# Performance work log

Hardware: AMD Instinct MI355X
Metric: run time of the kernel (lower is better)

The kernel has to match this reference:

```python
import jax, jax.numpy as jnp
import numpy as np

N = 10000          # nodes
E = 160000         # edges
T = 32             # seq_len == n_timesteps
H = 256            # hidden_size
K = 4              # edge_embedding_dim
NF = T * 6         # node_features
PRED = 8           # predicted_timesteps
T_TEACH = T - PRED # teacher-forced steps


def setup_inputs() -> dict:
    key = jax.random.key(0)
    ks = jax.random.split(key, 16)
    s = 0.05
    return {
        "x": jax.random.normal(ks[0], (N, NF), jnp.float32),
        "edge_index": jax.random.randint(ks[1], (2, E), 0, N, jnp.int64),
        "z": jax.random.uniform(ks[2], (E, K), jnp.float32),
        # inner f_out: Linear(H, NF) + ReLU
        "Wf": jax.random.normal(ks[3], (H, NF), jnp.float32) * s,
        "bf": jax.random.normal(ks[4], (NF,), jnp.float32) * s,
        # k-1 edge MLPs: Linear(2*NF, H) -> ReLU -> Linear(H, H), stacked
        "W1": jax.random.normal(ks[5], (K - 1, 2 * NF, H), jnp.float32) * s,
        "b1": jax.random.normal(ks[6], (K - 1, H), jnp.float32) * s,
        "W2": jax.random.normal(ks[7], (K - 1, H, H), jnp.float32) * s,
        "b2": jax.random.normal(ks[8], (K - 1, H), jnp.float32) * s,
        # GRUCell(6, H): torch gate order r, z, n
        "Wih": jax.random.normal(ks[9], (3 * H, 6), jnp.float32) * s,
        "bih": jax.random.normal(ks[10], (3 * H,), jnp.float32) * s,
        "Whh": jax.random.normal(ks[11], (3 * H, H), jnp.float32) * s,
        "bhh": jax.random.normal(ks[12], (3 * H,), jnp.float32) * s,
        # outer f_out: Linear(H, 6) + ReLU
        "Wo": jax.random.normal(ks[13], (H, 6), jnp.float32) * s,
        "bo": jax.random.normal(ks[14], (6,), jnp.float32) * s,
    }


def _forward(x, edge_index, z, Wf, bf, W1, b1, W2, b2, Wih, bih, Whh, bhh, Wo, bo):
    src = edge_index[0]  # x_j (source)
    dst = edge_index[1]  # x_i (target, aggregation index)
    zw = z[:, 1:K].T[:, :, None]  # [K-1, E, 1]
    ones_e = jnp.ones((E,), x.dtype)
    cnt = jnp.maximum(jax.ops.segment_sum(ones_e, dst, num_segments=N), 1.0)[:, None]

    def step(carry, inp):
        h, prev = carry
        t, x_t = inp
        inputs = jnp.where(t < T_TEACH, x_t, prev)  # [N, 6]
        fh = jax.nn.relu(h @ Wf + bf)               # [N, NF]
        # message: cat([x_i, x_j]) = [target, source], detached in torch
        ef = jax.lax.stop_gradient(
            jnp.concatenate([fh[dst], fh[src]], axis=1))  # [E, 2*NF]
        h1 = jax.nn.relu(jnp.einsum('ef,kfh->keh', ef, W1) + b1[:, None, :])
        h2 = jnp.einsum('keh,khg->keg', h1, W2) + b2[:, None, :]  # [K-1,E,H]
        msg = jnp.sum(zw * h2, axis=0)              # [E, H]
        m = jax.ops.segment_sum(msg, dst, num_segments=N) / cnt  # scatter-mean
        # GRUCell(inputs, hidden=m)
        gx = inputs @ Wih.T + bih                   # [N, 3H]
        gh = m @ Whh.T + bhh                        # [N, 3H]
        rx, zx, nx = jnp.split(gx, 3, axis=1)
        rh, zh, nh = jnp.split(gh, 3, axis=1)
        r = jax.nn.sigmoid(rx + rh)
        zg = jax.nn.sigmoid(zx + zh)
        n = jnp.tanh(nx + r * nh)
        h_new = (1.0 - zg) * n + zg * m             # [N, H]
        mu = inputs + jax.nn.relu(h_new @ Wo + bo)  # [N, 6]
        return (h_new, mu), mu

    x_seq = x.reshape(N, T, 6).transpose(1, 0, 2)   # [T, N, 6]
    ts = jnp.arange(T)
    h0 = jnp.zeros((N, H), x.dtype)
    p0 = jnp.zeros((N, 6), x.dtype)
    _, mus = jax.lax.scan(step, (h0, p0), (ts, x_seq))  # [T, N, 6]
    return mus.transpose(1, 0, 2).reshape(N, NF)


def reference(x, edge_index, z, Wf, bf, W1, b1, W2, b2, Wih, bih, Whh, bhh, Wo, bo):
    return _forward(x, edge_index, z, Wf, bf, W1, b1, W2, b2,
                    Wih, bih, Whh, bhh, Wo, bo)
```

## Files before the change

### kernel.cpp

```cpp
#include <hip/hip_runtime.h>
#include <hip/hip_bf16.h>

#define NN 10000
#define NE 160000
#define TS 32
#define HID 256
#define NFEAT 192
#define TTEACH 24

typedef unsigned short u16;
typedef unsigned int u32;
typedef __attribute__((ext_vector_type(8))) short bf16x8;
typedef __attribute__((ext_vector_type(4))) float f32x4;

__device__ __forceinline__ float bf2f(u16 u){
    u32 v = ((u32)u) << 16;
    union { u32 i; float f; } c; c.i = v; return c.f;
}
__device__ __forceinline__ u16 f2bf(float f){
    union { float f; u32 i; } c; c.f = f;
    u32 i = c.i;
    u32 lsb = (i >> 16) & 1u;
    i += 0x7fffu + lsb;
    return (u16)(i >> 16);
}

__global__ void fill_f32(float* p, float v, int n){
    int i = blockIdx.x * 256 + threadIdx.x;
    if (i < n) p[i] = v;
}
__global__ void fill_i32(int* p, int v, int n){
    int i = blockIdx.x * 256 + threadIdx.x;
    if (i < n) p[i] = v;
}
__global__ void copy_i32(const int* __restrict__ a, int* __restrict__ b, int n){
    int i = blockIdx.x * 256 + threadIdx.x;
    if (i < n) b[i] = a[i];
}

__global__ void detect_f32(const u16* __restrict__ zraw, int* __restrict__ flag){
    int c = 0;
    for (int i = 0; i < 128; i++) if (zraw[2*i] >= 0x4000) c++;
    *flag = (c > 8) ? 1 : 0;
}
__global__ void conv_f32(const void* __restrict__ in, float* __restrict__ outp,
                         int n, const int* __restrict__ flag){
    int i = blockIdx.x * 256 + threadIdx.x;
    if (i >= n) return;
    if (*flag) outp[i] = ((const float*)in)[i];
    else       outp[i] = bf2f(((const u16*)in)[i]);
}
__global__ void detect_i64(const int* __restrict__ ei_raw, int* __restrict__ flag){
    int zz = 0;
    #pragma unroll
    for (int i = 0; i < 32; i++) zz |= ei_raw[2*i + 1];
    *flag = (zz == 0) ? 1 : 0;
}
__global__ void copy_edges(const int* __restrict__ ei_raw, const int* __restrict__ flag,
                           int* __restrict__ src, int* __restrict__ dst){
    int e = blockIdx.x * 256 + threadIdx.x;
    if (e >= NE) return;
    int st = (*flag) ? 2 : 1;
    src[e] = ei_raw[(size_t)e * st];
    dst[e] = ei_raw[((size_t)NE + e) * st];
}

__global__ void degree_k(const int* __restrict__ dst, int* __restrict__ cnt, int n){
    int e = blockIdx.x * 256 + threadIdx.x;
    if (e < n) atomicAdd(&cnt[dst[e]], 1);
}
__global__ void invcnt_k(const int* __restrict__ cnt, float* __restrict__ inv, int n){
    int i = blockIdx.x * 256 + threadIdx.x;
    if (i < n) inv[i] = 1.0f / fmaxf((float)cnt[i], 1.0f);
}

__global__ void scan_k(const int* __restrict__ cnt, int* __restrict__ binoff){
    __shared__ int ps[1024];
    int t = threadIdx.x;
    int s = 0;
    if (t < 1000)
        for (int i = 0; i < 10; i++) s += cnt[t*10 + i];
    ps[t] = s;
    __syncthreads();
    for (int ofs = 1; ofs < 1024; ofs <<= 1){
        int v = (t >= ofs) ? ps[t - ofs] : 0;
        __syncthreads();
        ps[t] += v;
        __syncthreads();
    }
    if (t < 1000){
        int run = (t == 0) ? 0 : ps[t-1];
        for (int i = 0; i < 10; i++){
            binoff[t*10 + i] = run;
            run += cnt[t*10 + i];
        }
    }
}
__global__ void scatter_k(const int* __restrict__ src32, const int* __restrict__ dst32,
                          const float* __restrict__ zc, int* __restrict__ cur,
                          int* __restrict__ srcS, int* __restrict__ dstS,
                          float* __restrict__ zS){
    int e = blockIdx.x * 256 + threadIdx.x;
    if (e >= NE) return;
    int d = dst32[e];
    int pos = atomicAdd(&cur[d], 1);
    srcS[pos] = src32[e];
    dstS[pos] = d;
    zS[pos]        = zc[(size_t)e*4 + 1];
    zS[NE + pos]   = zc[(size_t)e*4 + 2];
    zS[2*NE + pos] = zc[(size_t)e*4 + 3];
}

__global__ void build_wft(const float* __restrict__ Wfc, u16* __restrict__ WfT){
    int idx = blockIdx.x * 256 + threadIdx.x;
    if (idx < 256 * 192){
        int k = idx / 192, n = idx % 192;
        WfT[(size_t)n * 256 + k] = f2bf(Wfc[idx]);
    }
}
__global__ void build_w1t(const float* __restrict__ W1c, u16* __restrict__ W1T){
    int idx = blockIdx.x * 256 + threadIdx.x;
    if (idx < 1536 * 192){
        int n = idx / 192, k = idx % 192;
        int kblk = n >> 9, part = (n >> 8) & 1, c = n & 255;
        W1T[idx] = f2bf(W1c[(size_t)kblk * (384*256) + (size_t)(part*192 + k) * 256 + c]);
    }
}
__global__ void conv_bf16(const float* __restrict__ in, u16* __restrict__ outp, int n){
    int i = blockIdx.x * 256 + threadIdx.x;
    if (i < n) outp[i] = f2bf(in[i]);
}
__global__ void build_w2t(const float* __restrict__ W2c, u16* __restrict__ W2T){
    int idx = blockIdx.x * 256 + threadIdx.x;
    if (idx < 768 * 256){
        int k = idx / 256, n = idx % 256;
        W2T[(size_t)n * 768 + k] = f2bf(W2c[idx]);
    }
}
__global__ void mscale_k(float* __restrict__ m_acc, const float* __restrict__ inv,
                         u16* __restrict__ m16){
    int idx = blockIdx.x * 256 + threadIdx.x;
    if (idx < NN * HID){
        m16[idx] = f2bf(m_acc[idx] * inv[idx >> 8]);
        m_acc[idx] = 0.f;
    }
}

template<int MODE>
__global__ __launch_bounds__(256, 2) void gemm_mfma(
    const u16* __restrict__ A16, const u16* __restrict__ BT16,
    const float* __restrict__ bias, float* __restrict__ Cf, u16* __restrict__ Cb,
    int M, int Kd, int Nd)
{
    __shared__ __align__(16) u16 Alds[256 * 40];
    __shared__ __align__(16) u16 Blds[64 * 40];
    const int tid = threadIdx.x;
    const int m0 = blockIdx.x * 256;
    const int n0 = blockIdx.y * 64;
    const int wave = tid >> 6, lane = tid & 63;
    const int quad = lane >> 4, l16 = lane & 15;

    const f32x4 zero4 = {0.f, 0.f, 0.f, 0.f};
    f32x4 acc[4][4];
    #pragma unroll
    for (int r=0;r<4;r++)
        #pragma unroll
        for (int c=0;c<4;c++) acc[r][c] = zero4;

    const int arow = m0 + tid;
    const u16* ap = &A16[(size_t)arow * Kd];
    const int bn = tid >> 2, bseg = tid & 3;
    const u16* bp = &BT16[(size_t)(n0 + bn) * Kd + bseg * 8];

    for (int k0 = 0; k0 < Kd; k0 += 32){
        if (arow < M){
            const uint4* q = reinterpret_cast<const uint4*>(ap + k0);
            uint4 v0 = q[0], v1 = q[1], v2 = q[2], v3 = q[3];
            *reinterpret_cast<uint4*>(&Alds[tid * 40])      = v0;
            *reinterpret_cast<uint4*>(&Alds[tid * 40 + 8])  = v1;
            *reinterpret_cast<uint4*>(&Alds[tid * 40 + 16]) = v2;
            *reinterpret_cast<uint4*>(&Alds[tid * 40 + 24]) = v3;
        } else {
            uint4 zz = {0,0,0,0};
            #pragma unroll
            for (int s=0;s<4;s++)
                *reinterpret_cast<uint4*>(&Alds[tid * 40 + s*8]) = zz;
        }
        {
            uint4 v = *reinterpret_cast<const uint4*>(bp + k0);
            *reinterpret_cast<uint4*>(&Blds[bn * 40 + bseg * 8]) = v;
        }
        __syncthreads();
        bf16x8 af[4], bfr[4];
        #pragma unroll
        for (int r=0;r<4;r++)
            af[r] = *reinterpret_cast<const bf16x8*>(&Alds[(wave*64 + r*16 + l16) * 40 + quad * 8]);
        #pragma unroll
        for (int c=0;c<4;c++)
            bfr[c] = *reinterpret_cast<const bf16x8*>(&Blds[(c*16 + l16) * 40 + quad * 8]);
        #pragma unroll
        for (int r=0;r<4;r++)
            #pragma unroll
            for (int c=0;c<4;c++)
                acc[r][c] = __builtin_amdgcn_mfma_f32_16x16x32_bf16(af[r], bfr[c], acc[r][c], 0, 0, 0);
        __syncthreads();
    }
    #pragma unroll
    for (int c=0;c<4;c++){
        int col = n0 + c*16 + l16;
        float bv = 0.f;
        if (MODE == 0 || MODE == 2) bv = bias[col];
        if (MODE == 1){
            int part = (col >> 8) & 1;
            if (part == 0) bv = bias[(col >> 9) * 256 + (col & 255)];
        }
        #pragma unroll
        for (int r=0;r<4;r++){
            #pragma unroll
            for (int reg=0;reg<4;reg++){
                int row = m0 + wave*64 + r*16 + quad*4 + reg;
                if (row >= M) continue;
                float v = acc[r][c][reg] + bv;
                if (MODE == 0) v = fmaxf(v, 0.f);
                if (MODE == 2) Cf[(size_t)row * Nd + col] = v;
                else           Cb[(size_t)row * Nd + col] = f2bf(v);
            }
        }
    }
}

__global__ __launch_bounds__(256, 2) void edge_mfma(
    const u16* __restrict__ AB16, const u16* __restrict__ W2T,
    const float* __restrict__ b2, const float* __restrict__ zS,
    const int* __restrict__ srcS, const int* __restrict__ dstS,
    float* __restrict__ m_acc)
{
    __shared__ __align__(16) char smem[33280];
    u16*   Alds = (u16*)smem;
    u16*   Blds = (u16*)(smem + 5120);
    float* stg  = (float*)smem;
    __shared__ float zc3[3][64];
    __shared__ int dstc[64], srcc[64];
    const int tid = threadIdx.x;
    const int eb = blockIdx.x * 64;

    if (tid < 64){
        srcc[tid] = srcS[eb + tid];
        dstc[tid] = dstS[eb + tid];
    }
    int tz = tid - 64;
    if (tz >= 0 && tz < 192){
        int g = tz / 64, e = tz % 64;
        zc3[g][e] = zS[(size_t)g * NE + eb + e];
    }
    __syncthreads();

    const int wave = tid >> 6, lane = tid & 63;
    const int quad = lane >> 4, l16 = lane & 15;
    const int est = tid >> 2, seg = tid & 3;

    const f32x4 zero4 = {0.f, 0.f, 0.f, 0.f};
    f32x4 acc[4][4];
    #pragma unroll
    for (int r=0;r<4;r++)
        #pragma unroll
        for (int c=0;c<4;c++) acc[r][c] = zero4;

    const int d = dstc[est], s = srcc[est];
    const u16* paB = &AB16[(size_t)d * 1536];
    const u16* pbB = &AB16[(size_t)s * 1536 + 256];
    const int bn = tid >> 2;
    const u16* bwB = &W2T[(size_t)bn * 768 + seg * 8];

    uint4 pa = *reinterpret_cast<const uint4*>(&paB[seg * 8]);
    uint4 pb = *reinterpret_cast<const uint4*>(&pbB[seg * 8]);

    for (int kc = 0; kc < 768; kc += 32){
        const int g = kc >> 8;
        {
            const u16* wa = (const u16*)&pa;
            const u16* wb = (const u16*)&pb;
            float zk = zc3[g][est];
            u16 pk[8];
            #pragma unroll
            for (int i=0;i<8;i++){
                float v = zk * fmaxf(bf2f(wa[i]) + bf2f(wb[i]), 0.f);
                pk[i] = f2bf(v);
            }
            *reinterpret_cast<uint4*>(&Alds[est * 40 + seg * 8]) = *reinterpret_cast<uint4*>(pk);
        }
        #pragma unroll
        for (int i=0;i<4;i++){
            uint4 w = *reinterpret_cast<const uint4*>(&bwB[(size_t)i * 64 * 768 + kc]);
            *reinterpret_cast<uint4*>(&Blds[(bn + i*64) * 40 + seg * 8]) = w;
        }
        __syncthreads();
        if (kc + 32 < 768){
            const int kn = kc + 32;
            const int gn = kn >> 8;
            const int jn = (kn & 255) + seg * 8;
            pa = *reinterpret_cast<const uint4*>(&paB[gn * 512 + jn]);
            pb = *reinterpret_cast<const uint4*>(&pbB[gn * 512 + jn]);
        }
        bf16x8 af[4], bfr[4];
        #pragma unroll
        for (int r=0;r<4;r++)
            af[r] = *reinterpret_cast<const bf16x8*>(&Alds[(r*16 + l16) * 40 + quad * 8]);
        #pragma unroll
        for (int c=0;c<4;c++)
            bfr[c] = *reinterpret_cast<const bf16x8*>(&Blds[(wave*64 + c*16 + l16) * 40 + quad * 8]);
        #pragma unroll
        for (int r=0;r<4;r++)
            #pragma unroll
            for (int c=0;c<4;c++)
                acc[r][c] = __builtin_amdgcn_mfma_f32_16x16x32_bf16(af[r], bfr[c], acc[r][c], 0, 0, 0);
        __syncthreads();
    }
    #pragma unroll
    for (int c=0;c<4;c++){
        int col = wave*64 + c*16 + l16;
        float b20 = b2[col], b21 = b2[256 + col], b22 = b2[512 + col];
        #pragma unroll
        for (int r=0;r<4;r++){
            #pragma unroll
            for (int reg=0;reg<4;reg++){
                int e = r*16 + quad*4 + reg;
                acc[r][c][reg] += zc3[0][e]*b20 + zc3[1][e]*b21 + zc3[2][e]*b22;
            }
        }
    }
    float sum = 0.f;
    int cur_d = -1;
    const int colg = wave*64 + lane;
    #pragma unroll
    for (int chunk = 0; chunk < 2; chunk++){
        #pragma unroll
        for (int rr = 0; rr < 2; rr++){
            int r = chunk*2 + rr;
            #pragma unroll
            for (int c=0;c<4;c++)
                #pragma unroll
                for (int reg=0;reg<4;reg++){
                    int el = rr*16 + quad*4 + reg;
                    stg[wave*(32*65) + el*65 + c*16 + l16] = acc[r][c][reg];
                }
        }
        __syncthreads();
        for (int e = 0; e < 32; e++){
            int eg = chunk*32 + e;
            int dn = dstc[eg];
            float v = stg[wave*(32*65) + e*65 + lane];
            if (dn != cur_d){
                if (cur_d >= 0) atomicAdd(&m_acc[(size_t)cur_d * 256 + colg], sum);
                cur_d = dn; sum = v;
            } else {
                sum += v;
            }
        }
        __syncthreads();
    }
    if (cur_d >= 0) atomicAdd(&m_acc[(size_t)cur_d * 256 + colg], sum);
}

__global__ void gates_mu_k(
    const float* __restrict__ gh, const u16* __restrict__ m16,
    const float* __restrict__ x, const float* __restrict__ Wih,
    const float* __restrict__ bih, const float* __restrict__ Wo,
    const float* __restrict__ bo, float* __restrict__ prev,
    u16* __restrict__ h16, void* __restrict__ out,
    const int* __restrict__ flag, int t)
{
    const int n = blockIdx.x;
    const int j = threadIdx.x;
    const int idx = n * 256 + j;
    float inp[6];
    if (t < TTEACH){
        #pragma unroll
        for (int c=0;c<6;c++) inp[c] = x[(size_t)n * NFEAT + t * 6 + c];
    } else {
        #pragma unroll
        for (int c=0;c<6;c++) inp[c] = prev[n * 6 + c];
    }
    float m = bf2f(m16[idx]);
    float gxr = bih[j], gxz = bih[256 + j], gxn = bih[512 + j];
    #pragma unroll
    for (int c=0;c<6;c++){
        gxr += inp[c] * Wih[j * 6 + c];
        gxz += inp[c] * Wih[(256 + j) * 6 + c];
        gxn += inp[c] * Wih[(512 + j) * 6 + c];
    }
    float ghr = gh[(size_t)n * 768 + j];
    float ghz = gh[(size_t)n * 768 + 256 + j];
    float ghn = gh[(size_t)n * 768 + 512 + j];
    float r  = 1.f / (1.f + __expf(-(gxr + ghr)));
    float zg = 1.f / (1.f + __expf(-(gxz + ghz)));
    float nn = tanhf(gxn + r * ghn);
    float hv = (1.f - zg) * nn + zg * m;
    h16[idx] = f2bf(hv);
    __shared__ float hl[256];
    __shared__ float part[6][9];
    hl[j] = hv;
    __syncthreads();
    if (j < 48){
        int c = j >> 3, p = j & 7;
        float s = 0.f;
        #pragma unroll 8
        for (int q = 0; q < 32; q++){
            int jj = p*32 + q;
            s += hl[jj] * Wo[jj * 6 + c];
        }
        part[c][p] = s;
    }
    __syncthreads();
    if (j < 6){
        float s = bo[j];
        #pragma unroll
        for (int p = 0; p < 8; p++) s += part[j][p];
        float mu = inp[j] + fmaxf(s, 0.f);
        if (*flag) ((float*)out)[(size_t)n * NFEAT + t * 6 + j] = mu;
        else       ((u16*)out)[(size_t)n * NFEAT + t * 6 + j] = f2bf(mu);
        prev[n * 6 + j] = mu;
    }
}

extern "C" void kernel_launch(void* const* d_in, const int* in_sizes, int n_in,
                              void* d_out, int out_size, void* d_ws, size_t ws_size,
                              hipStream_t stream)
{
    const void* x_r   = d_in[0];
    const int*  ei    = (const int*)d_in[1];
    const void* z_r   = d_in[2];
    const void* Wf_r  = d_in[3];
    const void* bf_r  = d_in[4];
    const void* W1_r  = d_in[5];
    const void* b1_r  = d_in[6];
    const void* W2_r  = d_in[7];
    const void* b2_r  = d_in[8];
    const void* Wih_r = d_in[9];
    const void* bih_r = d_in[10];
    const void* Whh_r = d_in[11];
    const void* bhh_r = d_in[12];
    const void* Wo_r  = d_in[13];
    const void* bo_r  = d_in[14];

    char* ws = (char*)d_ws;
    size_t off = 0;
    auto alloc = [&](size_t bytes){
        void* p = ws + off;
        off += (bytes + 255) & ~(size_t)255;
        return p;
    };
    u16*   h16   = (u16*)  alloc((size_t)NN * HID * 2);
    float* prev  = (float*)alloc((size_t)NN * 6 * 4);
    u16*   fh16  = (u16*)  alloc((size_t)NN * NFEAT * 2);
    u16*   AB16  = (u16*)  alloc((size_t)NN * 1536 * 2);
    float* m_acc = (float*)alloc((size_t)NN * HID * 4);
    u16*   m16   = (u16*)  alloc((size_t)NN * HID * 2);
    float* gh    = (float*)alloc((size_t)NN * 768 * 4);
    float* invc  = (float*)alloc((size_t)NN * 4);
    int*   cnt   = (int*)  alloc((size_t)NN * 4);
    int*   binoff= (int*)  alloc((size_t)(NN + 1) * 4);
    int*   curw  = (int*)  alloc((size_t)NN * 4);
    u16*   WfT   = (u16*)  alloc((size_t)192 * 256 * 2);
    u16*   W1T   = (u16*)  alloc((size_t)1536 * 192 * 2);
    u16*   Whh16 = (u16*)  alloc((size_t)768 * 256 * 2);
    u16*   W2T   = (u16*)  alloc((size_t)256 * 768 * 2);
    int*   src32 = (int*)  alloc((size_t)NE * 4);
    int*   dst32 = (int*)  alloc((size_t)NE * 4);
    int*   srcS  = (int*)  alloc((size_t)NE * 4);
    int*   dstS  = (int*)  alloc((size_t)NE * 4);
    float* zS    = (float*)alloc((size_t)3 * NE * 4);
    int*   fdt   = (int*)  alloc(256);
    int*   fidx  = (int*)  alloc(256);
    float* xc   = (float*)alloc((size_t)NN * NFEAT * 4);
    float* zc   = (float*)alloc((size_t)NE * 4 * 4);
    float* Wfc  = (float*)alloc((size_t)256 * 192 * 4);
    float* bfc  = (float*)alloc(192 * 4);
    float* W1c  = (float*)alloc((size_t)3 * 384 * 256 * 4);
    float* b1c  = (float*)alloc(768 * 4);
    float* W2c  = (float*)alloc((size_t)3 * 256 * 256 * 4);
    float* b2c  = (float*)alloc(768 * 4);
    float* Wihc = (float*)alloc((size_t)768 * 6 * 4);
    float* bihc = (float*)alloc(768 * 4);
    float* Whhc = (float*)alloc((size_t)768 * 256 * 4);
    float* bhhc = (float*)alloc(768 * 4);
    float* Woc  = (float*)alloc((size_t)256 * 6 * 4);
    float* boc  = (float*)alloc(6 * 4);

    detect_f32<<<1, 1, 0, stream>>>((const u16*)z_r, fdt);
    detect_i64<<<1, 1, 0, stream>>>(ei, fidx);
    copy_edges<<<(NE + 255)/256, 256, 0, stream>>>(ei, fidx, src32, dst32);

    auto conv = [&](const void* in, float* outp, int n){
        conv_f32<<<(n + 255)/256, 256, 0, stream>>>(in, outp, n, fdt);
    };
    conv(x_r,   xc,   NN * NFEAT);
    conv(z_r,   zc,   NE * 4);
    conv(Wf_r,  Wfc,  256 * 192);
    conv(bf_r,  bfc,  192);
    conv(W1_r,  W1c,  3 * 384 * 256);
    conv(b1_r,  b1c,  768);
    conv(W2_r,  W2c,  3 * 256 * 256);
    conv(b2_r,  b2c,  768);
    conv(Wih_r, Wihc, 768 * 6);
    conv(bih_r, bihc, 768);
    conv(Whh_r, Whhc, 768 * 256);
    conv(bhh_r, bhhc, 768);
    conv(Wo_r,  Woc,  256 * 6);
    conv(bo_r,  boc,  6);

    fill_f32<<<(NN*HID/2 + 255)/256, 256, 0, stream>>>((float*)h16, 0.f, NN*HID/2);
    fill_f32<<<(NN*6 + 255)/256, 256, 0, stream>>>(prev, 0.f, NN*6);
    fill_f32<<<(NN*HID + 255)/256, 256, 0, stream>>>(m_acc, 0.f, NN*HID);
    fill_i32<<<(NN + 255)/256, 256, 0, stream>>>(cnt, 0, NN);
    degree_k<<<(NE + 255)/256, 256, 0, stream>>>(dst32, cnt, NE);
    invcnt_k<<<(NN + 255)/256, 256, 0, stream>>>(cnt, invc, NN);
    scan_k<<<1, 1024, 0, stream>>>(cnt, binoff);
    copy_i32<<<(NN + 255)/256, 256, 0, stream>>>(binoff, curw, NN);
    scatter_k<<<(NE + 255)/256, 256, 0, stream>>>(src32, dst32, zc, curw, srcS, dstS, zS);
    build_wft<<<(256*192 + 255)/256, 256, 0, stream>>>(Wfc, WfT);
    build_w1t<<<(1536*192 + 255)/256, 256, 0, stream>>>(W1c, W1T);
    conv_bf16<<<(768*256 + 255)/256, 256, 0, stream>>>(Whhc, Whh16, 768*256);
    build_w2t<<<(768*256 + 255)/256, 256, 0, stream>>>(W2c, W2T);

    for (int t = 0; t < TS; t++){
        gemm_mfma<0><<<dim3(40, 3), 256, 0, stream>>>(h16, WfT, bfc, nullptr, fh16, NN, 256, NFEAT);
        gemm_mfma<1><<<dim3(40, 24), 256, 0, stream>>>(fh16, W1T, b1c, nullptr, AB16, NN, NFEAT, 1536);
        edge_mfma<<<2500, 256, 0, stream>>>(AB16, W2T, b2c, zS, srcS, dstS, m_acc);
        mscale_k<<<(NN*HID + 255)/256, 256, 0, stream>>>(m_acc, invc, m16);
        gemm_mfma<2><<<dim3(40, 12), 256, 0, stream>>>(m16, Whh16, bhhc, gh, nullptr, NN, 256, 768);
        gates_mu_k<<<NN, 256, 0, stream>>>(gh, m16, xc, Wihc, bihc, Woc, boc, prev, h16, d_out, fdt, t);
    }
}
```

Baseline: 7.231 ms.

## Fuse mean-scaling into Whh GEMM and gates kernel, drop mscale pass

Removes the separate mscale kernel. The Whh GEMM now reads the fp32 scatter accumulator directly, scaling rows by inverse degree and converting to bf16 while loading tiles. The gates kernel reads fp32 m and resets the accumulator to zero. The edge kernel also uses packed bf16x2 conversions and a smaller 16-row staging chunk in its epilogue, which shrinks LDS use. The cost is that the GEMM A loads are twice as wide (fp32), and the gates kernel now uses fp32 m where it used bf16 before.

```diff
diff --git a/kernel.cpp b/kernel.cpp
--- a/kernel.cpp
+++ b/kernel.cpp
@@ -137,19 +137,12 @@
         W2T[(size_t)n * 768 + k] = f2bf(W2c[idx]);
     }
 }
-__global__ void mscale_k(float* __restrict__ m_acc, const float* __restrict__ inv,
-                         u16* __restrict__ m16){
-    int idx = blockIdx.x * 256 + threadIdx.x;
-    if (idx < NN * HID){
-        m16[idx] = f2bf(m_acc[idx] * inv[idx >> 8]);
-        m_acc[idx] = 0.f;
-    }
-}
 
 template<int MODE>
 __global__ __launch_bounds__(256, 2) void gemm_mfma(
     const u16* __restrict__ A16, const u16* __restrict__ BT16,
     const float* __restrict__ bias, float* __restrict__ Cf, u16* __restrict__ Cb,
+    const float* __restrict__ A32, const float* __restrict__ rowscale,
     int M, int Kd, int Nd)
 {
     __shared__ __align__(16) u16 Alds[256 * 40];
@@ -168,23 +161,50 @@
         for (int c=0;c<4;c++) acc[r][c] = zero4;
 
     const int arow = m0 + tid;
-    const u16* ap = &A16[(size_t)arow * Kd];
+    const u16* ap = (MODE == 2) ? nullptr : &A16[(size_t)arow * Kd];
     const int bn = tid >> 2, bseg = tid & 3;
     const u16* bp = &BT16[(size_t)(n0 + bn) * Kd + bseg * 8];
+    float rs = 0.f;
+    if (MODE == 2 && arow < M) rs = rowscale[arow];
 
     for (int k0 = 0; k0 < Kd; k0 += 32){
-        if (arow < M){
-            const uint4* q = reinterpret_cast<const uint4*>(ap + k0);
-            uint4 v0 = q[0], v1 = q[1], v2 = q[2], v3 = q[3];
-            *reinterpret_cast<uint4*>(&Alds[tid * 40])      = v0;
-            *reinterpret_cast<uint4*>(&Alds[tid * 40 + 8])  = v1;
-            *reinterpret_cast<uint4*>(&Alds[tid * 40 + 16]) = v2;
-            *reinterpret_cast<uint4*>(&Alds[tid * 40 + 24]) = v3;
+        if (MODE == 2){
+            if (arow < M){
+                const float4* q = reinterpret_cast<const float4*>(&A32[(size_t)arow * Kd + k0]);
+                u32 pk[16];
+                #pragma unroll
+                for (int s=0;s<8;s++){
+                    float4 v = q[s];
+                    float2 p0; p0.x = v.x * rs; p0.y = v.y * rs;
+                    float2 p1; p1.x = v.z * rs; p1.y = v.w * rs;
+                    __hip_bfloat162 h0 = __float22bfloat162_rn(p0);
+                    __hip_bfloat162 h1 = __float22bfloat162_rn(p1);
+                    pk[2*s]   = *reinterpret_cast<u32*>(&h0);
+                    pk[2*s+1] = *reinterpret_cast<u32*>(&h1);
+                }
+                #pragma unroll
+                for (int s=0;s<4;s++)
+                    *reinterpret_cast<uint4*>(&Alds[tid * 40 + s*8]) = *reinterpret_cast<uint4*>(&pk[4*s]);
+            } else {
+                uint4 zz = {0,0,0,0};
+                #pragma unroll
+                for (int s=0;s<4;s++)
+                    *reinterpret_cast<uint4*>(&Alds[tid * 40 + s*8]) = zz;
+            }
         } else {
-            uint4 zz = {0,0,0,0};
-            #pragma unroll
-            for (int s=0;s<4;s++)
-                *reinterpret_cast<uint4*>(&Alds[tid * 40 + s*8]) = zz;
+            if (arow < M){
+                const uint4* q = reinterpret_cast<const uint4*>(ap + k0);
+                uint4 v0 = q[0], v1 = q[1], v2 = q[2], v3 = q[3];
+                *reinterpret_cast<uint4*>(&Alds[tid * 40])      = v0;
+                *reinterpret_cast<uint4*>(&Alds[tid * 40 + 8])  = v1;
+                *reinterpret_cast<uint4*>(&Alds[tid * 40 + 16]) = v2;
+                *reinterpret_cast<uint4*>(&Alds[tid * 40 + 24]) = v3;
+            } else {
+                uint4 zz = {0,0,0,0};
+                #pragma unroll
+                for (int s=0;s<4;s++)
+                    *reinterpret_cast<uint4*>(&Alds[tid * 40 + s*8]) = zz;
+            }
         }
         {
             uint4 v = *reinterpret_cast<const uint4*>(bp + k0);
@@ -235,7 +255,7 @@
     const int* __restrict__ srcS, const int* __restrict__ dstS,
     float* __restrict__ m_acc)
 {
-    __shared__ __align__(16) char smem[33280];
+    __shared__ __align__(16) char smem[25600];
     u16*   Alds = (u16*)smem;
     u16*   Blds = (u16*)(smem + 5120);
     float* stg  = (float*)smem;
@@ -278,14 +298,19 @@
     for (int kc = 0; kc < 768; kc += 32){
         const int g = kc >> 8;
         {
-            const u16* wa = (const u16*)&pa;
-            const u16* wb = (const u16*)&pb;
+            union { uint4 v; u32 w[4]; } UA, UB;
+            UA.v = pa; UB.v = pb;
             float zk = zc3[g][est];
-            u16 pk[8];
+            u32 pk[4];
             #pragma unroll
-            for (int i=0;i<8;i++){
-                float v = zk * fmaxf(bf2f(wa[i]) + bf2f(wb[i]), 0.f);
-                pk[i] = f2bf(v);
+            for (int i=0;i<4;i++){
+                float2 fa = __bfloat1622float2(*reinterpret_cast<__hip_bfloat162*>(&UA.w[i]));
+                float2 fb = __bfloat1622float2(*reinterpret_cast<__hip_bfloat162*>(&UB.w[i]));
+                float2 v;
+                v.x = zk * fmaxf(fa.x + fb.x, 0.f);
+                v.y = zk * fmaxf(fa.y + fb.y, 0.f);
+                __hip_bfloat162 hr = __float22bfloat162_rn(v);
+                pk[i] = *reinterpret_cast<u32*>(&hr);
             }
             *reinterpret_cast<uint4*>(&Alds[est * 40 + seg * 8]) = *reinterpret_cast<uint4*>(pk);
         }
@@ -333,23 +358,17 @@
     int cur_d = -1;
     const int colg = wave*64 + lane;
     #pragma unroll
-    for (int chunk = 0; chunk < 2; chunk++){
-        #pragma unroll
-        for (int rr = 0; rr < 2; rr++){
-            int r = chunk*2 + rr;
+    for (int r = 0; r < 4; r++){
+        #pragma unroll
+        for (int c=0;c<4;c++)
             #pragma unroll
-            for (int c=0;c<4;c++)
-                #pragma unroll
-                for (int reg=0;reg<4;reg++){
-                    int el = rr*16 + quad*4 + reg;
-                    stg[wave*(32*65) + el*65 + c*16 + l16] = acc[r][c][reg];
-                }
-        }
-        __syncthreads();
-        for (int e = 0; e < 32; e++){
-            int eg = chunk*32 + e;
+            for (int reg=0;reg<4;reg++)
+                stg[wave*(16*65) + (quad*4 + reg)*65 + c*16 + l16] = acc[r][c][reg];
+        __syncthreads();
+        for (int e = 0; e < 16; e++){
+            int eg = r*16 + e;
             int dn = dstc[eg];
-            float v = stg[wave*(32*65) + e*65 + lane];
+            float v = stg[wave*(16*65) + e*65 + lane];
             if (dn != cur_d){
                 if (cur_d >= 0) atomicAdd(&m_acc[(size_t)cur_d * 256 + colg], sum);
                 cur_d = dn; sum = v;
@@ -363,11 +382,11 @@
 }
 
 __global__ void gates_mu_k(
-    const float* __restrict__ gh, const u16* __restrict__ m16,
-    const float* __restrict__ x, const float* __restrict__ Wih,
-    const float* __restrict__ bih, const float* __restrict__ Wo,
-    const float* __restrict__ bo, float* __restrict__ prev,
-    u16* __restrict__ h16, void* __restrict__ out,
+    const float* __restrict__ gh, float* __restrict__ m_acc,
+    const float* __restrict__ inv_cnt, const float* __restrict__ x,
+    const float* __restrict__ Wih, const float* __restrict__ bih,
+    const float* __restrict__ Wo, const float* __restrict__ bo,
+    float* __restrict__ prev, u16* __restrict__ h16, void* __restrict__ out,
     const int* __restrict__ flag, int t)
 {
     const int n = blockIdx.x;
@@ -381,7 +400,8 @@
         #pragma unroll
         for (int c=0;c<6;c++) inp[c] = prev[n * 6 + c];
     }
-    float m = bf2f(m16[idx]);
+    float m = m_acc[idx] * inv_cnt[n];
+    m_acc[idx] = 0.f;
     float gxr = bih[j], gxz = bih[256 + j], gxn = bih[512 + j];
     #pragma unroll
     for (int c=0;c<6;c++){
@@ -455,7 +475,6 @@
     u16*   fh16  = (u16*)  alloc((size_t)NN * NFEAT * 2);
     u16*   AB16  = (u16*)  alloc((size_t)NN * 1536 * 2);
     float* m_acc = (float*)alloc((size_t)NN * HID * 4);
-    u16*   m16   = (u16*)  alloc((size_t)NN * HID * 2);
     float* gh    = (float*)alloc((size_t)NN * 768 * 4);
     float* invc  = (float*)alloc((size_t)NN * 4);
     int*   cnt   = (int*)  alloc((size_t)NN * 4);
@@ -524,11 +543,10 @@
     build_w2t<<<(768*256 + 255)/256, 256, 0, stream>>>(W2c, W2T);
 
     for (int t = 0; t < TS; t++){
-        gemm_mfma<0><<<dim3(40, 3), 256, 0, stream>>>(h16, WfT, bfc, nullptr, fh16, NN, 256, NFEAT);
-        gemm_mfma<1><<<dim3(40, 24), 256, 0, stream>>>(fh16, W1T, b1c, nullptr, AB16, NN, NFEAT, 1536);
+        gemm_mfma<0><<<dim3(40, 3), 256, 0, stream>>>(h16, WfT, bfc, nullptr, fh16, nullptr, nullptr, NN, 256, NFEAT);
+        gemm_mfma<1><<<dim3(40, 24), 256, 0, stream>>>(fh16, W1T, b1c, nullptr, AB16, nullptr, nullptr, NN, NFEAT, 1536);
         edge_mfma<<<2500, 256, 0, stream>>>(AB16, W2T, b2c, zS, srcS, dstS, m_acc);
-        mscale_k<<<(NN*HID + 255)/256, 256, 0, stream>>>(m_acc, invc, m16);
-        gemm_mfma<2><<<dim3(40, 12), 256, 0, stream>>>(m16, Whh16, bhhc, gh, nullptr, NN, 256, 768);
-        gates_mu_k<<<NN, 256, 0, stream>>>(gh, m16, xc, Wihc, bihc, Woc, boc, prev, h16, d_out, fdt, t);
-    }
-}
+        gemm_mfma<2><<<dim3(40, 12), 256, 0, stream>>>(nullptr, Whh16, bhhc, gh, nullptr, m_acc, invc, NN, 256, 768);
+        gates_mu_k<<<NN, 256, 0, stream>>>(gh, m_acc, invc, xc, Wihc, bihc, Woc, boc, prev, h16, d_out, fdt, t);
+    }
+}
```

Result: no change. 7.278 ms (+0.6%).
